# Kernel optimization log

Measured on AMD Instinct MI355X. Metric: run time of the kernel, lower is better.

Reference implementation:

```python
import jax, jax.numpy as jnp
import numpy as np

KERNEL_MUL = 2.0
KERNEL_NUM = 5


def setup_inputs() -> dict:
    key = jax.random.key(0)
    k1, k2 = jax.random.split(key)
    source = jax.random.normal(k1, (4096, 256), dtype=jnp.float32)
    target = jax.random.normal(k2, (4096, 256), dtype=jnp.float32)
    return {"source": source, "target": target}


def reference(source, target):
    B = source.shape[0]
    total = jnp.concatenate([source, target], axis=0)  # [2N, D]
    n = total.shape[0]
    # Pairwise squared L2 distances via ||a||^2 + ||b||^2 - 2 a.b (same math,
    # avoids the O(n^2 * D) expanded intermediate of the torch code).
    sq = jnp.sum(total * total, axis=-1)  # [2N]
    L2 = sq[:, None] + sq[None, :] - 2.0 * (total @ total.T)  # [2N, 2N]
    L2 = jnp.maximum(L2, 0.0)  # exact distances are non-negative
    # bandwidth uses L2_distance.data in torch -> stop_gradient here
    bandwidth = jax.lax.stop_gradient(jnp.sum(L2)) / (n * n - n)
    bandwidth = bandwidth / (KERNEL_MUL ** (KERNEL_NUM // 2))
    kernels = jnp.zeros_like(L2)
    for i in range(KERNEL_NUM):
        bw = bandwidth * (KERNEL_MUL ** i) + 1e-9
        kernels = kernels + jnp.exp(-L2 / bw)
    xx = jnp.mean(kernels[:B, :B])
    yy = jnp.mean(kernels[B:, B:])
    xy = jnp.mean(kernels[:B, B:])
    yx = jnp.mean(kernels[B:, :B])
    loss = xx + yy - xy - yx  # == mean(XX + YY - XY - YX) since blocks are BxB
    return (loss, jnp.max(L2), xx, yy, xy, yx)
```

## Files before the change

### kernel.cpp

```cpp
#include <hip/hip_runtime.h>
#include <math.h>


constexpr int NTOT  = 8192;
constexpr int BHALF = 4096;
constexpr int DIM   = 256;
constexpr int BM    = 128;

typedef __attribute__((ext_vector_type(8))) short bf16x8;
typedef __attribute__((ext_vector_type(4))) float f32x4;

#define GLOAD_LDS16(gp, lp)                                                      \
    __builtin_amdgcn_global_load_lds(                                            \
        (__attribute__((address_space(1))) const void*)(gp),                     \
        (__attribute__((address_space(3))) void*)(lp), 16, 0, 0)


__device__ __forceinline__ int swz(int row, int byteInRow) {
    return (row * 128 + byteInRow) ^ ((row & 7) << 4);
}

__device__ __forceinline__ unsigned short rne_bf16(float f) {
    unsigned u = __float_as_uint(f);
    return (unsigned short)((u + 0x7fffu + ((u >> 16) & 1u)) >> 16);
}

__global__ __launch_bounds__(256) void prep_kernel(
        const float* __restrict__ src, const float* __restrict__ tgt,
        float* __restrict__ sq, double* __restrict__ vcol,
        unsigned short* __restrict__ hi) {
    __shared__ float cs[4][256];
    const int t = threadIdx.x;
    const int w = t >> 6, l = t & 63;
    const int seg = l >> 4;
    const int b8  = (l * 8) & 127;
    float c0 = 0.f, c1 = 0.f, c2 = 0.f, c3 = 0.f;

#pragma unroll
    for (int it = 0; it < 8; ++it) {
        const int row = blockIdx.x * 32 + w * 8 + it;
        const float* p = (row < BHALF) ? src + (size_t)row * DIM
                                       : tgt + (size_t)(row - BHALF) * DIM;
        float4 v = reinterpret_cast<const float4*>(p)[l];
        float s = v.x * v.x + v.y * v.y + v.z * v.z + v.w * v.w;
#pragma unroll
        for (int off = 32; off; off >>= 1) s += __shfl_down(s, off);
        if (l == 0) sq[row] = s;
        c0 += v.x; c1 += v.y; c2 += v.z; c3 += v.w;

        unsigned hp0 = (unsigned)rne_bf16(v.x) | ((unsigned)rne_bf16(v.y) << 16);
        unsigned hp1 = (unsigned)rne_bf16(v.z) | ((unsigned)rne_bf16(v.w) << 16);
        const size_t byteoff = (size_t)row * 512 + seg * 128 + (b8 ^ ((row & 7) << 4));
        *reinterpret_cast<uint2*>((char*)hi + byteoff) = make_uint2(hp0, hp1);
    }

    cs[w][l * 4 + 0] = c0; cs[w][l * 4 + 1] = c1;
    cs[w][l * 4 + 2] = c2; cs[w][l * 4 + 3] = c3;
    __syncthreads();
    float tot = cs[0][t] + cs[1][t] + cs[2][t] + cs[3][t];
    atomicAdd(&vcol[t], (double)tot);
}

__global__ void bw_kernel(const float* __restrict__ sq,
                          const double* __restrict__ v,
                          float* __restrict__ bwp) {
    __shared__ double red[256];
    int t = threadIdx.x;
    double s = 0.0;
    for (int i = t; i < NTOT; i += 256) s += (double)sq[i];
    red[t] = s; __syncthreads();
    for (int off = 128; off; off >>= 1) {
        if (t < off) red[t] += red[t + off];
        __syncthreads();
    }
    double S1 = red[0];
    __syncthreads();
    double d = v[t];
    red[t] = d * d; __syncthreads();
    for (int off = 128; off; off >>= 1) {
        if (t < off) red[t] += red[t + off];
        __syncthreads();
    }
    if (t == 0) {
        double V2 = red[0];
        const double n = (double)NTOT;
        double sumL2 = 2.0 * n * S1 - 2.0 * V2;
        *bwp = (float)(sumL2 / (n * n - n) / 4.0);
    }
}

__global__ __launch_bounds__(256, 4) void gram_kernel(
        const unsigned short* __restrict__ hi,
        const float* __restrict__ sq, const float* __restrict__ bwp,
        double* __restrict__ qsum, int* __restrict__ maxBits) {
    const int tb = blockIdx.x;
    const int id = (tb & 7) * 260 + (tb >> 3);
    int k = 2079 - id;
    int u = (int)((sqrt((double)(8 * k + 1)) - 1.0) * 0.5);
    while ((u + 1) * (u + 2) / 2 <= k) ++u;
    while (u * (u + 1) / 2 > k) --u;
    const int by = 63 - u;
    const int bx = 63 - (k - u * (u + 1) / 2);
    const bool diag = (bx == by);

    __shared__ alignas(16) char ldsA[BM * 128];
    __shared__ alignas(16) char ldsB[BM * 128];
    __shared__ double sred[4];
    __shared__ float  mred[4];

    const int i0 = by * BM;
    const int j0 = bx * BM;
    const char* Ahi = (const char*)hi + (size_t)i0 * 512;
    const char* Bhi = (const char*)hi + (size_t)j0 * 512;

    const int t    = threadIdx.x;
    const int lane = t & 63;
    const int w    = t >> 6;
    const int wr   = w >> 1;
    const int wc   = w & 1;
    const int lrow = lane & 15;

    f32x4 acc[4][4] = {};

    for (int seg = 0; seg < 4; ++seg) {
#pragma unroll
        for (int it = 0; it < 4; ++it) {
            const int chunk = it * 4 + w;
            const int o     = chunk * 1024 + lane * 16;
            const int row   = o >> 7;
            const size_t srcoff = (size_t)row * 512 + seg * 128 + (o & 127);
            GLOAD_LDS16(Ahi + srcoff, ldsA + chunk * 1024);
            if (!diag) GLOAD_LDS16(Bhi + srcoff, ldsB + chunk * 1024);
        }
        __syncthreads();

        const char* bbuf = diag ? ldsA : ldsB;
#pragma unroll
        for (int ks = 0; ks < 2; ++ks) {
            const int kb = ks * 64 + (lane >> 4) * 16;
            bf16x8 a[4], b[4];
#pragma unroll
            for (int mt = 0; mt < 4; ++mt)
                a[mt] = *reinterpret_cast<const bf16x8*>(
                    ldsA + swz(wr * 64 + mt * 16 + lrow, kb));
#pragma unroll
            for (int nt = 0; nt < 4; ++nt)
                b[nt] = *reinterpret_cast<const bf16x8*>(
                    bbuf + swz(wc * 64 + nt * 16 + lrow, kb));
#pragma unroll
            for (int mt = 0; mt < 4; ++mt)
#pragma unroll
                for (int nt = 0; nt < 4; ++nt)
                    acc[mt][nt] = __builtin_amdgcn_mfma_f32_16x16x32_bf16(
                        a[mt], b[nt], acc[mt][nt], 0, 0, 0);
        }
        __syncthreads();
    }

    const float bw = *bwp;
    const float L2E = 1.44269504088896340736f;
    float ic[5];
#pragma unroll
    for (int i = 0; i < 5; ++i) ic[i] = -L2E / (bw * (float)(1 << i) + 1e-9f);

    float m = 0.0f;
    float ksum = 0.0f;
    const int rbase = i0 + wr * 64 + (lane >> 4) * 4;
    const int cbase = j0 + wc * 64 + lrow;
    float sb[4];
#pragma unroll
    for (int nt = 0; nt < 4; ++nt) sb[nt] = sq[cbase + nt * 16];
#pragma unroll
    for (int mt = 0; mt < 4; ++mt) {
        float sa[4];
#pragma unroll
        for (int r = 0; r < 4; ++r) sa[r] = sq[rbase + mt * 16 + r];
#pragma unroll
        for (int nt = 0; nt < 4; ++nt)
#pragma unroll
            for (int r = 0; r < 4; ++r) {
                float l2 = fmaxf(sa[r] + sb[nt] - 2.0f * acc[mt][nt][r], 0.0f);
                m = fmaxf(m, l2);
                ksum += exp2f(l2 * ic[0]) + exp2f(l2 * ic[1]) + exp2f(l2 * ic[2])
                      + exp2f(l2 * ic[3]) + exp2f(l2 * ic[4]);
            }
    }

    double s = (double)ksum;
#pragma unroll
    for (int off = 32; off; off >>= 1) {
        s += __shfl_down(s, off);
        m  = fmaxf(m, __shfl_down(m, off));
    }
    if ((t & 63) == 0) { sred[w] = s; mred[w] = m; }
    __syncthreads();
    if (t == 0) {
        double st = sred[0] + sred[1] + sred[2] + sred[3];
        float  mt = fmaxf(fmaxf(mred[0], mred[1]), fmaxf(mred[2], mred[3]));
        atomicMax(maxBits, __float_as_int(mt));
        const int q  = (((i0 >= BHALF) ? 2 : 0) | ((j0 >= BHALF) ? 1 : 0));
        const int qT = (((j0 >= BHALF) ? 2 : 0) | ((i0 >= BHALF) ? 1 : 0));
        if (diag) {
            atomicAdd(&qsum[q], st);
        } else if (q == qT) {
            atomicAdd(&qsum[q], 2.0 * st);
        } else {
            atomicAdd(&qsum[q],  st);
            atomicAdd(&qsum[qT], st);
        }
    }
}

__global__ void final_kernel(const double* __restrict__ qsum,
                             const int* __restrict__ maxBits,
                             float* __restrict__ out) {
    const double denom = (double)BHALF * (double)BHALF;
    const double xx = qsum[0] / denom;
    const double xy = qsum[1] / denom;
    const double yx = qsum[2] / denom;
    const double yy = qsum[3] / denom;
    out[0] = (float)(xx + yy - xy - yx);
    out[1] = __int_as_float(*maxBits);
    out[2] = (float)xx;
    out[3] = (float)yy;
    out[4] = (float)xy;
    out[5] = (float)yx;
}

extern "C" void kernel_launch(void* const* d_in, const int* in_sizes, int n_in,
                              void* d_out, int out_size, void* d_ws, size_t ws_size,
                              hipStream_t stream) {
    const float* src = (const float*)d_in[0];
    const float* tgt = (const float*)d_in[1];
    float* out = (float*)d_out;

    double* qsum = (double*)d_ws;
    int*    maxB = (int*)   ((char*)d_ws + 32);
    float*  bwp  = (float*) ((char*)d_ws + 36);
    double* vcol = (double*)((char*)d_ws + 64);
    float*  sq   = (float*) ((char*)d_ws + 2112);
    unsigned short* hi = (unsigned short*)((char*)d_ws + 36864);

    hipMemsetAsync(d_ws, 0, 2112, stream);

    prep_kernel<<<NTOT / 32, 256, 0, stream>>>(src, tgt, sq, vcol, hi);
    bw_kernel<<<1, 256, 0, stream>>>(sq, vcol, bwp);
    gram_kernel<<<2080, 256, 0, stream>>>(hi, sq, bwp, qsum, maxB);
    final_kernel<<<1, 1, 0, stream>>>(qsum, maxB, out);
}
```

Baseline: 172.2 us.

## Compute multi-bandwidth kernel sum via repeated squaring and drop double atomics

The five exp2 evaluations per distance become a single exp2 at the widest bandwidth, followed by repeated squaring to get the narrower-bandwidth terms. The per-column sums in prep move from double atomicAdd to per-block partials that bw_kernel reduces serially, which also shrinks the memset. The gram kernel's launch bounds drop the minimum-4-blocks hint, letting the compiler use more registers at a possible cost in occupancy. Repeated squaring compounds rounding error and ignores the 1e-9 epsilon per bandwidth, so results may differ slightly.

```diff
diff --git a/kernel.cpp b/kernel.cpp
--- a/kernel.cpp
+++ b/kernel.cpp
@@ -27,7 +27,7 @@
 
 __global__ __launch_bounds__(256) void prep_kernel(
         const float* __restrict__ src, const float* __restrict__ tgt,
-        float* __restrict__ sq, double* __restrict__ vcol,
+        float* __restrict__ sq, float* __restrict__ colpart,
         unsigned short* __restrict__ hi) {
     __shared__ float cs[4][256];
     const int t = threadIdx.x;
@@ -57,12 +57,11 @@
     cs[w][l * 4 + 0] = c0; cs[w][l * 4 + 1] = c1;
     cs[w][l * 4 + 2] = c2; cs[w][l * 4 + 3] = c3;
     __syncthreads();
-    float tot = cs[0][t] + cs[1][t] + cs[2][t] + cs[3][t];
-    atomicAdd(&vcol[t], (double)tot);
+    colpart[blockIdx.x * 256 + t] = cs[0][t] + cs[1][t] + cs[2][t] + cs[3][t];
 }
 
 __global__ void bw_kernel(const float* __restrict__ sq,
-                          const double* __restrict__ v,
+                          const float* __restrict__ colpart,
                           float* __restrict__ bwp) {
     __shared__ double red[256];
     int t = threadIdx.x;
@@ -75,8 +74,9 @@
     }
     double S1 = red[0];
     __syncthreads();
-    double d = v[t];
-    red[t] = d * d; __syncthreads();
+    double v = 0.0;
+    for (int b = 0; b < 256; ++b) v += (double)colpart[b * 256 + t];
+    red[t] = v * v; __syncthreads();
     for (int off = 128; off; off >>= 1) {
         if (t < off) red[t] += red[t + off];
         __syncthreads();
@@ -89,7 +89,7 @@
     }
 }
 
-__global__ __launch_bounds__(256, 4) void gram_kernel(
+__global__ __launch_bounds__(256) void gram_kernel(
         const unsigned short* __restrict__ hi,
         const float* __restrict__ sq, const float* __restrict__ bwp,
         double* __restrict__ qsum, int* __restrict__ maxBits) {
@@ -157,11 +157,8 @@
         __syncthreads();
     }
 
-    const float bw = *bwp;
-    const float L2E = 1.44269504088896340736f;
-    float ic[5];
-#pragma unroll
-    for (int i = 0; i < 5; ++i) ic[i] = -L2E / (bw * (float)(1 << i) + 1e-9f);
+    const float bw  = *bwp;
+    const float ic4 = -1.44269504088896340736f / (bw * 16.0f + 1e-9f);
 
     float m = 0.0f;
     float ksum = 0.0f;
@@ -179,10 +176,14 @@
         for (int nt = 0; nt < 4; ++nt)
 #pragma unroll
             for (int r = 0; r < 4; ++r) {
-                float l2 = fmaxf(sa[r] + sb[nt] - 2.0f * acc[mt][nt][r], 0.0f);
+                float l2 = fmaxf(fmaf(-2.0f, acc[mt][nt][r], sa[r] + sb[nt]), 0.0f);
                 m = fmaxf(m, l2);
-                ksum += exp2f(l2 * ic[0]) + exp2f(l2 * ic[1]) + exp2f(l2 * ic[2])
-                      + exp2f(l2 * ic[3]) + exp2f(l2 * ic[4]);
+                float e1  = exp2f(l2 * ic4);
+                float e2  = e1 * e1;
+                float e4  = e2 * e2;
+                float e8  = e4 * e4;
+                float e16 = e8 * e8;
+                ksum += (e1 + e2) + (e4 + e8) + e16;
             }
     }
 
@@ -234,17 +235,17 @@
     const float* tgt = (const float*)d_in[1];
     float* out = (float*)d_out;
 
-    double* qsum = (double*)d_ws;
-    int*    maxB = (int*)   ((char*)d_ws + 32);
-    float*  bwp  = (float*) ((char*)d_ws + 36);
-    double* vcol = (double*)((char*)d_ws + 64);
-    float*  sq   = (float*) ((char*)d_ws + 2112);
+    double* qsum    = (double*)d_ws;
+    int*    maxB    = (int*)   ((char*)d_ws + 32);
+    float*  bwp     = (float*) ((char*)d_ws + 36);
+    float*  sq      = (float*) ((char*)d_ws + 2112);
     unsigned short* hi = (unsigned short*)((char*)d_ws + 36864);
-
-    hipMemsetAsync(d_ws, 0, 2112, stream);
-
-    prep_kernel<<<NTOT / 32, 256, 0, stream>>>(src, tgt, sq, vcol, hi);
-    bw_kernel<<<1, 256, 0, stream>>>(sq, vcol, bwp);
+    float*  colpart = (float*) ((char*)d_ws + 36864 + (size_t)NTOT * DIM * 2);
+
+    hipMemsetAsync(d_ws, 0, 64, stream);
+
+    prep_kernel<<<NTOT / 32, 256, 0, stream>>>(src, tgt, sq, colpart, hi);
+    bw_kernel<<<1, 256, 0, stream>>>(sq, colpart, bwp);
     gram_kernel<<<2080, 256, 0, stream>>>(hi, sq, bwp, qsum, maxB);
     final_kernel<<<1, 1, 0, stream>>>(qsum, maxB, out);
 }
```

After: 158.9 us. 7.7% less time.
